# Performance work log

Measured on AMD Instinct MI355X. Metric: run time of the kernel, lower is better.

Reference implementation:

```python
import jax, jax.numpy as jnp
import numpy as np

# ---- constants derived exactly as in CQCCExtractor.__init__ ----
SR = 16000
FMIN = 32.7
N_BINS = 96
BINS_OCT = 24
N_CQCC = 20
HOP = 128
Q = 1.0 / (2.0 ** (1.0 / BINS_OCT) - 1.0)
MIN_WIN = max(16, int(Q * SR / FMIN))          # 16699
N_FFT = 1
while N_FFT < MIN_WIN * 2:
    N_FFT <<= 1                                # 65536
NUM_FREQ = N_FFT // 2 + 1                      # 32769


def _dct_mat():
    k = np.arange(N_CQCC)[:, None]
    n = np.arange(N_BINS)[None, :]
    return jnp.asarray(np.cos(np.pi * k * (2 * n + 1) / (2 * N_BINS)), dtype=jnp.float32)


def _delta(feat, N=2):
    # vectorized version of the per-frame python loop: d[t] = sum_n n*(f[min(t+n,T-1)] - f[max(t-n,0)]) / denom
    denom = 2 * sum(i * i for i in range(1, N + 1))
    T = feat.shape[0]
    p = jnp.concatenate([jnp.repeat(feat[:1], N, axis=0), feat, jnp.repeat(feat[-1:], N, axis=0)], axis=0)
    num = sum(n * (p[N + n:N + n + T] - p[N - n:N - n + T]) for n in range(1, N + 1))
    return num / denom


def setup_inputs() -> dict:
    key = jax.random.key(0)
    wav = jax.random.normal(key, (262144,), dtype=jnp.float32)
    return {"wav": wav}


def reference(wav) -> jnp.ndarray:
    # periodic hann window of length MIN_WIN, zero-padded (centered) to N_FFT like torch.stft
    w = 0.5 - 0.5 * jnp.cos(2.0 * jnp.pi * jnp.arange(MIN_WIN, dtype=jnp.float32) / MIN_WIN)
    left = (N_FFT - MIN_WIN) // 2
    win = jnp.zeros((N_FFT,), dtype=jnp.float32).at[left:left + MIN_WIN].set(w)

    # torch.stft(center=True, pad_mode='reflect')
    pad = N_FFT // 2
    x = jnp.pad(wav, pad, mode='reflect')
    n_frames = 1 + wav.shape[0] // HOP
    starts = jnp.arange(n_frames) * HOP
    frames = x[starts[:, None] + jnp.arange(N_FFT)[None, :]] * win      # [T, n_fft]
    spec = jnp.fft.rfft(frames, axis=-1)                                 # [T, F] complex64
    power = jnp.abs(spec) ** 2                                           # [T, F]

    # linear interpolation of STFT power at geometrically spaced CQT freqs
    cqt_freqs = FMIN * 2.0 ** (jnp.arange(N_BINS, dtype=jnp.float32) / BINS_OCT)
    idx_float = cqt_freqs / (SR / 2) * (NUM_FREQ - 1)
    idx_lo = jnp.clip(idx_float.astype(jnp.int32), 0, NUM_FREQ - 2)
    idx_hi = idx_lo + 1
    alpha = (idx_float - idx_lo.astype(jnp.float32))                     # [n_bins]
    cqt_power = (1.0 - alpha) * power[:, idx_lo] + alpha * power[:, idx_hi]  # [T, n_bins]

    log_cqt = jnp.log(jnp.maximum(cqt_power, 1e-8))
    cqcc = log_cqt @ _dct_mat().T                                        # [T, n_cqcc]
    # normalize over time (torch.std default is unbiased, ddof=1)
    cqcc = (cqcc - cqcc.mean(axis=0)) / (jnp.std(cqcc, axis=0, ddof=1) + 1e-8)

    d1 = _delta(cqcc)
    d2 = _delta(d1)
    return jnp.concatenate([cqcc, d1, d2], axis=-1)                      # [T, 3*n_cqcc]
```

## Files before the change

### kernel.cpp

```cpp
#include <hip/hip_runtime.h>
#include <math.h>

#define WAV_N     262144
#define HOP       128
#define MIN_WIN   16699
#define LEFT      24418
#define T_FRAMES  2049
#define N_BINS    96
#define N_CQCC    20
#define F_COMP    192
#define NF        576
#define NBLK      2179
#define NBP       2240
#define PARTLEN   59
#define FULLBLK   130
#define XS_VALID  278843
#define TWOPI     6.283185307179586f

#define BT   16
#define FTW  64
#define AST  20

#define WS_QFP  0
#define WS_V    20643840
#define WS_CQ   30117888
#define WS_SUMS 30281808
#define VTP     2056

__device__ __forceinline__ void f_to_fi_sigma(int f, int& fi, int& sigma) {
    int plane = f / 192;
    int c = f - plane * 192;
    int bin = c >> 1, hi = c & 1;
    float e    = (float)bin / 24.0f;
    float fb   = 32.7f * exp2f(e);
    float idxf = fb / 8000.0f * 32768.0f;
    fi = (int)idxf + hi;
    sigma = (plane == 0) ? 0 : (plane == 1 ? 1 : -1);
}

__device__ __forceinline__ void make_rot(int fi, int sg, float& Dr, float& Di) {
    float fr = (float)fi * (1.0f / 65536.0f) - (float)sg * (1.0f / (float)MIN_WIN);
    fr -= rintf(fr);
    float sn, cs; __sincosf(TWOPI * fr, &sn, &cs);
    Dr = cs; Di = -sn;
}

#define STEP(a0_, a1_, a2_, a3_) do {                                   \
    xr[0] = fmaf((a0_), Wr, xr[0]); xi[0] = fmaf((a0_), Wi, xi[0]);     \
    xr[1] = fmaf((a1_), Wr, xr[1]); xi[1] = fmaf((a1_), Wi, xi[1]);     \
    xr[2] = fmaf((a2_), Wr, xr[2]); xi[2] = fmaf((a2_), Wi, xi[2]);     \
    xr[3] = fmaf((a3_), Wr, xr[3]); xi[3] = fmaf((a3_), Wi, xi[3]);     \
    float wr_ = Wr;                                                     \
    Wr = wr_ * Dr - Wi * Di;                                            \
    Wi = wr_ * Di + Wi * Dr; } while (0)

__global__ __launch_bounds__(256) void k_chunk(const float* __restrict__ wav,
                                               float4* __restrict__ QFP) {
    __shared__ __align__(16) float A_lds[128 * AST];
    int tid = threadIdx.x;
    int b0 = blockIdx.x * BT;
    int f0 = blockIdx.y * FTW;

    {
        int sbase = 128 * b0;
        #pragma unroll
        for (int k = 0; k < 8; ++k) {
            int m = k * 256 + tid;
            int j = m & 127, bl = m >> 7;
            int s = sbase + m;
            float v = 0.0f;
            if (s < XS_VALID) {
                int w = s - 8350;
                if (w < 0) w = -w;
                if (w >= WAV_N) w = 2 * WAV_N - 2 - w;
                v = wav[w];
            }
            A_lds[j * AST + bl] = v;
        }
    }

    int fl = tid & 63;
    int bg = tid >> 6;
    int bl0 = bg * 4;
    int bb = b0 + bl0;

    int f = f0 + fl;
    int fi, sg; f_to_fi_sigma(f, fi, sg);
    float Dr, Di; make_rot(fi, sg, Dr, Di);
    float Wr = 1.0f, Wi = 0.0f;

    float xr[4] = {0, 0, 0, 0}, xi[4] = {0, 0, 0, 0};
    float pr[4], pi[4];

    __syncthreads();

    #pragma unroll 4
    for (int j = 0; j < PARTLEN; ++j) {
        float4 a = *(const float4*)&A_lds[j * AST + bl0];
        STEP(a.x, a.y, a.z, a.w);
    }
    #pragma unroll
    for (int i = 0; i < 4; ++i) { pr[i] = xr[i]; pi[i] = xi[i]; }
    #pragma unroll 4
    for (int j = PARTLEN; j < 128; ++j) {
        float4 a = *(const float4*)&A_lds[j * AST + bl0];
        STEP(a.x, a.y, a.z, a.w);
    }

    float4* dst = QFP + (size_t)f * NBP + bb;
    #pragma unroll
    for (int i = 0; i < 4; ++i) {
        int b = bb + i;
        unsigned ph = ((unsigned)fi * (unsigned)(LEFT + 128 * b)) & 65535u;
        float frf = (float)ph * (1.0f / 65536.0f)
                  - (float)sg * (float)((128 * b) % MIN_WIN) * (1.0f / (float)MIN_WIN);
        frf -= rintf(frf);
        float sn, cs; __sincosf(TWOPI * frf, &sn, &cs);
        dst[i] = make_float4(xr[i] * cs + xi[i] * sn,
                             xi[i] * cs - xr[i] * sn,
                             pr[i] * cs + pi[i] * sn,
                             pi[i] * cs - pr[i] * sn);
    }
}

#define SEG 5
__global__ __launch_bounds__(512) void k_scan(const float4* __restrict__ QFP,
                                              float2* __restrict__ V,
                                              double* __restrict__ sums) {
    __shared__ float4 col[NBLK];
    __shared__ double2 wsum[8];
    int tid = threadIdx.x;
    int f = blockIdx.x;
    if (f == 0 && tid < 40) sums[tid] = 0.0;

    const float4* g = QFP + (size_t)f * NBP;
    #pragma unroll
    for (int k = 0; k < SEG; ++k) {
        int idx = k * 512 + tid;
        if (idx < NBLK) col[idx] = g[idx];
    }
    __syncthreads();

    int s0 = tid * SEG, s1 = min(s0 + SEG, NBLK);
    double sr = 0.0, si = 0.0;
    for (int i = s0; i < s1; ++i) { sr += col[i].x; si += col[i].y; }
    double r = sr, im = si;
    #pragma unroll
    for (int off = 1; off < 64; off <<= 1) {
        double prx = __shfl_up(r, off);
        double piy = __shfl_up(im, off);
        if ((tid & 63) >= off) { r += prx; im += piy; }
    }
    if ((tid & 63) == 63) wsum[tid >> 6] = make_double2(r, im);
    __syncthreads();
    double basr = 0.0, basi = 0.0;
    int w = tid >> 6;
    for (int ww = 0; ww < w; ++ww) { basr += wsum[ww].x; basi += wsum[ww].y; }
    double gr = basr + r - sr, gi = basi + im - si;
    for (int i = s0; i < s1; ++i) {
        float qx = col[i].x, qy = col[i].y;
        col[i].x = (float)gr; col[i].y = (float)gi;
        gr += qx; gi += qy;
    }
    __syncthreads();

    int fi_, sg_; f_to_fi_sigma(f, fi_, sg_);
    float2* vrow = V + (size_t)f * VTP;
    #pragma unroll
    for (int k = 0; k < SEG; ++k) {
        int t = k * 512 + tid;
        if (t < T_FRAMES) {
            float4 ca = col[t];
            float4 cb = col[t + FULLBLK];
            float ur = cb.x - ca.x + cb.z;
            float ui = cb.y - ca.y + cb.w;
            unsigned ph = ((unsigned)fi_ * 128u * (unsigned)t) & 65535u;
            float frf = (float)ph * (1.0f / 65536.0f)
                      - (float)sg_ * (float)((128 * t) % MIN_WIN) * (1.0f / (float)MIN_WIN);
            frf -= rintf(frf);
            float sn, cs;
            __sincosf(TWOPI * frf, &sn, &cs);
            vrow[t] = make_float2(ur * cs - ui * sn, ur * sn + ui * cs);
        }
    }
}

#define TF 8
__global__ __launch_bounds__(256) void k_cqt(const float2* __restrict__ V,
                                             float* __restrict__ cq,
                                             double* __restrict__ sums) {
    __shared__ float dctm[N_CQCC * N_BINS];
    __shared__ float2 sc[F_COMP * TF];
    __shared__ float lg[N_BINS * TF];
    __shared__ float cqv[N_CQCC * TF];
    int tid = threadIdx.x;
    int tb = blockIdx.x * TF;
    for (int idx = tid; idx < N_CQCC * N_BINS; idx += 256) {
        int k = idx / N_BINS, b = idx - k * N_BINS;
        dctm[idx] = cosf((float)M_PI * (float)(k * (2 * b + 1)) / 192.0f);
    }
    for (int idx = tid; idx < F_COMP * TF; idx += 256) {
        int c = idx / TF, tl = idx % TF;
        int t = tb + tl;
        float2 v = make_float2(0.f, 0.f);
        if (t < T_FRAMES) {
            float2 v0 = V[(size_t)c * VTP + t];
            float2 v1 = V[(size_t)(192 + c) * VTP + t];
            float2 v2 = V[(size_t)(384 + c) * VTP + t];
            v = make_float2(0.5f * v0.x - 0.25f * (v1.x + v2.x),
                            0.5f * v0.y - 0.25f * (v1.y + v2.y));
        }
        sc[idx] = v;
    }
    __syncthreads();
    for (int idx = tid; idx < N_BINS * TF; idx += 256) {
        int b = idx / TF, tl = idx % TF;
        float2 lo = sc[(2 * b) * TF + tl];
        float2 hi = sc[(2 * b + 1) * TF + tl];
        float pl = lo.x * lo.x + lo.y * lo.y;
        float ph = hi.x * hi.x + hi.y * hi.y;
        float e    = (float)b / 24.0f;
        float fb   = 32.7f * exp2f(e);
        float idxf = fb / 8000.0f * 32768.0f;
        float alpha = idxf - (float)((int)idxf);
        float p = (1.0f - alpha) * pl + alpha * ph;
        lg[idx] = logf(fmaxf(p, 1e-8f));
    }
    __syncthreads();
    for (int idx = tid; idx < N_CQCC * TF; idx += 256) {
        int k = idx / TF, tl = idx % TF;
        int t = tb + tl;
        float s = 0.0f;
        #pragma unroll 4
        for (int b = 0; b < N_BINS; ++b) s += dctm[k * N_BINS + b] * lg[b * TF + tl];
        cqv[idx] = (t < T_FRAMES) ? s : 0.0f;
        if (t < T_FRAMES) cq[t * N_CQCC + k] = s;
    }
    __syncthreads();
    if (tid < N_CQCC) {
        double s1 = 0.0, s2 = 0.0;
        #pragma unroll
        for (int tl = 0; tl < TF; ++tl) {
            if (tb + tl < T_FRAMES) {
                double v = (double)cqv[tid * TF + tl];
                s1 += v; s2 += v * v;
            }
        }
        atomicAdd(&sums[tid], s1);
        atomicAdd(&sums[N_CQCC + tid], s2);
    }
}

__device__ __forceinline__ int clampT(int v) {
    return v < 0 ? 0 : (v > T_FRAMES - 1 ? T_FRAMES - 1 : v);
}

__global__ void k_final(const float* __restrict__ cq, const double* __restrict__ sums,
                        float* __restrict__ out) {
    int gid = blockIdx.x * blockDim.x + threadIdx.x;
    if (gid >= T_FRAMES * N_CQCC) return;
    int t = gid / N_CQCC;
    int k = gid - t * N_CQCC;
    double S1 = sums[k], S2 = sums[N_CQCC + k];
    double md = S1 / (double)T_FRAMES;
    double var = (S2 - S1 * md) / (double)(T_FRAMES - 1);
    double sd = sqrt(var > 0.0 ? var : 0.0);
    float m = (float)md;
    float iv = (float)(1.0 / (sd + 1e-8));
    float cv[9];
    #pragma unroll
    for (int j = 0; j < 9; ++j)
        cv[j] = (cq[clampT(t + j - 4) * N_CQCC + k] - m) * iv;
    float dv[5];
    #pragma unroll
    for (int o = -2; o <= 2; ++o) {
        int p = clampT(t + o);
        int h1 = clampT(p + 1) - t, l1 = clampT(p - 1) - t;
        int h2 = clampT(p + 2) - t, l2 = clampT(p - 2) - t;
        dv[o + 2] = ((cv[h1 + 4] - cv[l1 + 4]) + 2.0f * (cv[h2 + 4] - cv[l2 + 4])) * 0.1f;
    }
    out[t * 60 + k]      = cv[4];
    out[t * 60 + 20 + k] = dv[2];
    out[t * 60 + 40 + k] = (dv[3] - dv[1] + 2.0f * (dv[4] - dv[0])) * 0.1f;
}

extern "C" void kernel_launch(void* const* d_in, const int* in_sizes, int n_in,
                              void* d_out, int out_size, void* d_ws, size_t ws_size,
                              hipStream_t stream) {
    const float* wav = (const float*)d_in[0];
    float* out = (float*)d_out;
    char* ws = (char*)d_ws;
    float4* QFP  = (float4*)(ws + WS_QFP);
    float2* V    = (float2*)(ws + WS_V);
    float*  cq   = (float*)(ws + WS_CQ);
    double* sums = (double*)(ws + WS_SUMS);

    k_chunk<<<dim3(NBP / BT, NF / FTW), 256, 0, stream>>>(wav, QFP);
    k_scan<<<NF, 512, 0, stream>>>(QFP, V, sums);
    k_cqt<<<(T_FRAMES + TF - 1) / TF, 256, 0, stream>>>(V, cq, sums);
    k_final<<<(T_FRAMES * N_CQCC + 255) / 256, 256, 0, stream>>>(cq, sums, out);
}
```

Baseline: 103.4 us.

## Split chunk DFT into four phase-strided accumulators and precompute DCT matrix once

The per-sample twiddle recurrence in k_chunk is replaced by four interleaved accumulator sets that share one twiddle advanced by D^4. The four sets are then combined with D, D^2 and D^3 at the partial point and at the end. This shortens the serial complex-rotate dependency chain per sample, at the cost of more registers. The DCT cosine table is now computed once by one k_chunk block and written to workspace, so every k_cqt block no longer recomputes cosf.

```diff
diff --git a/kernel.cpp b/kernel.cpp
--- a/kernel.cpp
+++ b/kernel.cpp
@@ -25,6 +25,7 @@
 #define WS_V    20643840
 #define WS_CQ   30117888
 #define WS_SUMS 30281808
+#define WS_DCT  30282368
 #define VTP     2056
 
 __device__ __forceinline__ void f_to_fi_sigma(int f, int& fi, int& sigma) {
@@ -45,17 +46,9 @@
     Dr = cs; Di = -sn;
 }
 
-#define STEP(a0_, a1_, a2_, a3_) do {                                   \
-    xr[0] = fmaf((a0_), Wr, xr[0]); xi[0] = fmaf((a0_), Wi, xi[0]);     \
-    xr[1] = fmaf((a1_), Wr, xr[1]); xi[1] = fmaf((a1_), Wi, xi[1]);     \
-    xr[2] = fmaf((a2_), Wr, xr[2]); xi[2] = fmaf((a2_), Wi, xi[2]);     \
-    xr[3] = fmaf((a3_), Wr, xr[3]); xi[3] = fmaf((a3_), Wi, xi[3]);     \
-    float wr_ = Wr;                                                     \
-    Wr = wr_ * Dr - Wi * Di;                                            \
-    Wi = wr_ * Di + Wi * Dr; } while (0)
-
 __global__ __launch_bounds__(256) void k_chunk(const float* __restrict__ wav,
-                                               float4* __restrict__ QFP) {
+                                               float4* __restrict__ QFP,
+                                               float* __restrict__ dct_g) {
     __shared__ __align__(16) float A_lds[128 * AST];
     int tid = threadIdx.x;
     int b0 = blockIdx.x * BT;
@@ -87,39 +80,111 @@
     int f = f0 + fl;
     int fi, sg; f_to_fi_sigma(f, fi, sg);
     float Dr, Di; make_rot(fi, sg, Dr, Di);
+    float D2r = Dr * Dr - Di * Di,    D2i = 2.0f * Dr * Di;
+    float D3r = D2r * Dr - D2i * Di,  D3i = D2r * Di + D2i * Dr;
+    float D4r = D2r * D2r - D2i * D2i, D4i = 2.0f * D2r * D2i;
     float Wr = 1.0f, Wi = 0.0f;
 
-    float xr[4] = {0, 0, 0, 0}, xi[4] = {0, 0, 0, 0};
+    float s0r[4] = {0,0,0,0}, s0i[4] = {0,0,0,0};
+    float s1r[4] = {0,0,0,0}, s1i[4] = {0,0,0,0};
+    float s2r[4] = {0,0,0,0}, s2i[4] = {0,0,0,0};
+    float s3r[4] = {0,0,0,0}, s3i[4] = {0,0,0,0};
     float pr[4], pi[4];
 
     __syncthreads();
 
-    #pragma unroll 4
-    for (int j = 0; j < PARTLEN; ++j) {
-        float4 a = *(const float4*)&A_lds[j * AST + bl0];
-        STEP(a.x, a.y, a.z, a.w);
-    }
-    #pragma unroll
-    for (int i = 0; i < 4; ++i) { pr[i] = xr[i]; pi[i] = xi[i]; }
-    #pragma unroll 4
-    for (int j = PARTLEN; j < 128; ++j) {
-        float4 a = *(const float4*)&A_lds[j * AST + bl0];
-        STEP(a.x, a.y, a.z, a.w);
+    #define STEP4(a_, b_, c_, d_) do {                                        \
+        const float aa_[4] = {(a_).x, (a_).y, (a_).z, (a_).w};                \
+        const float bb_[4] = {(b_).x, (b_).y, (b_).z, (b_).w};                \
+        const float cc_[4] = {(c_).x, (c_).y, (c_).z, (c_).w};                \
+        const float dd_[4] = {(d_).x, (d_).y, (d_).z, (d_).w};                \
+        _Pragma("unroll")                                                     \
+        for (int i = 0; i < 4; ++i) {                                         \
+            s0r[i] = fmaf(aa_[i], Wr, s0r[i]); s0i[i] = fmaf(aa_[i], Wi, s0i[i]); \
+            s1r[i] = fmaf(bb_[i], Wr, s1r[i]); s1i[i] = fmaf(bb_[i], Wi, s1i[i]); \
+            s2r[i] = fmaf(cc_[i], Wr, s2r[i]); s2i[i] = fmaf(cc_[i], Wi, s2i[i]); \
+            s3r[i] = fmaf(dd_[i], Wr, s3r[i]); s3i[i] = fmaf(dd_[i], Wi, s3i[i]); \
+        }                                                                     \
+        float wr_ = Wr;                                                       \
+        Wr = wr_ * D4r - Wi * D4i;                                            \
+        Wi = wr_ * D4i + Wi * D4r; } while (0)
+
+    #define COMBINE(rr_, ii_, i_) do {                                        \
+        float t1r = fmaf(Dr,  s1r[i_], fmaf(-Di,  s1i[i_], s0r[i_]));         \
+        float t1i = fmaf(Dr,  s1i[i_], fmaf( Di,  s1r[i_], s0i[i_]));         \
+        float t2r = fmaf(D2r, s2r[i_], fmaf(-D2i, s2i[i_], t1r));             \
+        float t2i = fmaf(D2r, s2i[i_], fmaf( D2i, s2r[i_], t1i));             \
+        rr_ = fmaf(D3r, s3r[i_], fmaf(-D3i, s3i[i_], t2r));                   \
+        ii_ = fmaf(D3r, s3i[i_], fmaf( D3i, s3r[i_], t2i)); } while (0)
+
+    #pragma unroll 1
+    for (int m = 0; m < 14; ++m) {
+        float4 a = *(const float4*)&A_lds[(4 * m    ) * AST + bl0];
+        float4 b = *(const float4*)&A_lds[(4 * m + 1) * AST + bl0];
+        float4 c = *(const float4*)&A_lds[(4 * m + 2) * AST + bl0];
+        float4 d = *(const float4*)&A_lds[(4 * m + 3) * AST + bl0];
+        STEP4(a, b, c, d);
+    }
+    {
+        float4 a = *(const float4*)&A_lds[56 * AST + bl0];
+        float4 b = *(const float4*)&A_lds[57 * AST + bl0];
+        float4 c = *(const float4*)&A_lds[58 * AST + bl0];
+        const float aa_[4] = {a.x, a.y, a.z, a.w};
+        const float bb_[4] = {b.x, b.y, b.z, b.w};
+        const float cc_[4] = {c.x, c.y, c.z, c.w};
+        #pragma unroll
+        for (int i = 0; i < 4; ++i) {
+            s0r[i] = fmaf(aa_[i], Wr, s0r[i]); s0i[i] = fmaf(aa_[i], Wi, s0i[i]);
+            s1r[i] = fmaf(bb_[i], Wr, s1r[i]); s1i[i] = fmaf(bb_[i], Wi, s1i[i]);
+            s2r[i] = fmaf(cc_[i], Wr, s2r[i]); s2i[i] = fmaf(cc_[i], Wi, s2i[i]);
+        }
+    }
+    #pragma unroll
+    for (int i = 0; i < 4; ++i) COMBINE(pr[i], pi[i], i);
+    {
+        float4 d = *(const float4*)&A_lds[59 * AST + bl0];
+        const float dd_[4] = {d.x, d.y, d.z, d.w};
+        #pragma unroll
+        for (int i = 0; i < 4; ++i) {
+            s3r[i] = fmaf(dd_[i], Wr, s3r[i]); s3i[i] = fmaf(dd_[i], Wi, s3i[i]);
+        }
+        float wr_ = Wr;
+        Wr = wr_ * D4r - Wi * D4i;
+        Wi = wr_ * D4i + Wi * D4r;
+    }
+    #pragma unroll 1
+    for (int m = 15; m < 32; ++m) {
+        float4 a = *(const float4*)&A_lds[(4 * m    ) * AST + bl0];
+        float4 b = *(const float4*)&A_lds[(4 * m + 1) * AST + bl0];
+        float4 c = *(const float4*)&A_lds[(4 * m + 2) * AST + bl0];
+        float4 d = *(const float4*)&A_lds[(4 * m + 3) * AST + bl0];
+        STEP4(a, b, c, d);
     }
 
     float4* dst = QFP + (size_t)f * NBP + bb;
     #pragma unroll
     for (int i = 0; i < 4; ++i) {
+        float qr, qi;
+        COMBINE(qr, qi, i);
         int b = bb + i;
         unsigned ph = ((unsigned)fi * (unsigned)(LEFT + 128 * b)) & 65535u;
         float frf = (float)ph * (1.0f / 65536.0f)
                   - (float)sg * (float)((128 * b) % MIN_WIN) * (1.0f / (float)MIN_WIN);
         frf -= rintf(frf);
         float sn, cs; __sincosf(TWOPI * frf, &sn, &cs);
-        dst[i] = make_float4(xr[i] * cs + xi[i] * sn,
-                             xi[i] * cs - xr[i] * sn,
+        dst[i] = make_float4(qr * cs + qi * sn,
+                             qi * cs - qr * sn,
                              pr[i] * cs + pi[i] * sn,
                              pi[i] * cs - pr[i] * sn);
+    }
+    #undef STEP4
+    #undef COMBINE
+
+    if (blockIdx.x == 0 && blockIdx.y == 0) {
+        for (int idx = tid; idx < N_CQCC * N_BINS; idx += 256) {
+            int k = idx / N_BINS, b = idx - k * N_BINS;
+            dct_g[idx] = cosf((float)M_PI * (float)(k * (2 * b + 1)) / 192.0f);
+        }
     }
 }
 
@@ -187,6 +252,7 @@
 
 #define TF 8
 __global__ __launch_bounds__(256) void k_cqt(const float2* __restrict__ V,
+                                             const float* __restrict__ dct_g,
                                              float* __restrict__ cq,
                                              double* __restrict__ sums) {
     __shared__ float dctm[N_CQCC * N_BINS];
@@ -195,10 +261,8 @@
     __shared__ float cqv[N_CQCC * TF];
     int tid = threadIdx.x;
     int tb = blockIdx.x * TF;
-    for (int idx = tid; idx < N_CQCC * N_BINS; idx += 256) {
-        int k = idx / N_BINS, b = idx - k * N_BINS;
-        dctm[idx] = cosf((float)M_PI * (float)(k * (2 * b + 1)) / 192.0f);
-    }
+    for (int idx = tid; idx < N_CQCC * N_BINS; idx += 256)
+        dctm[idx] = dct_g[idx];
     for (int idx = tid; idx < F_COMP * TF; idx += 256) {
         int c = idx / TF, tl = idx % TF;
         int t = tb + tl;
@@ -294,9 +358,10 @@
     float2* V    = (float2*)(ws + WS_V);
     float*  cq   = (float*)(ws + WS_CQ);
     double* sums = (double*)(ws + WS_SUMS);
-
-    k_chunk<<<dim3(NBP / BT, NF / FTW), 256, 0, stream>>>(wav, QFP);
+    float*  dct  = (float*)(ws + WS_DCT);
+
+    k_chunk<<<dim3(NBP / BT, NF / FTW), 256, 0, stream>>>(wav, QFP, dct);
     k_scan<<<NF, 512, 0, stream>>>(QFP, V, sums);
-    k_cqt<<<(T_FRAMES + TF - 1) / TF, 256, 0, stream>>>(V, cq, sums);
+    k_cqt<<<(T_FRAMES + TF - 1) / TF, 256, 0, stream>>>(V, dct, cq, sums);
     k_final<<<(T_FRAMES * N_CQCC + 255) / 256, 256, 0, stream>>>(cq, sums, out);
 }
```

Result: faster. 100.5 us (-2.7%).
